# Kernel optimization log

Hardware: AMD Instinct MI355X
Metric: run time of the kernel (lower is better)

## Reference

```python
import jax, jax.numpy as jnp
import numpy as np

N_NODES = 100000
N_EDGES = 1600000
IN_CH, HID, OUT_CH = 512, 32, 64


def setup_inputs() -> dict:
    key = jax.random.key(0)
    ks = jax.random.split(key, 8)
    x = jax.random.normal(ks[0], (N_NODES, IN_CH), dtype=jnp.float32)
    edge_index = jax.random.randint(ks[1], (2, N_EDGES), 0, N_NODES, dtype=jnp.int64)
    def glorot(k, fan_in, fan_out):
        lim = np.sqrt(6.0 / (fan_in + fan_out)).astype(np.float32)
        return jax.random.uniform(k, (fan_in, fan_out), jnp.float32, -lim, lim)
    return {
        "x": x,
        "edge_index": edge_index,
        "W1": glorot(ks[2], IN_CH, HID), "b1": jnp.zeros((HID,), jnp.float32),
        "W2": glorot(ks[3], HID, HID),   "b2": jnp.zeros((HID,), jnp.float32),
        "W3": glorot(ks[4], HID, OUT_CH),"b3": jnp.zeros((OUT_CH,), jnp.float32),
    }


def _gcn_norm(edge_index, n_nodes):
    # PyG GCNConv: add self-loops, symmetric normalization D^-1/2 (A+I) D^-1/2
    loops = jnp.arange(n_nodes, dtype=edge_index.dtype)
    src = jnp.concatenate([edge_index[0], loops])
    dst = jnp.concatenate([edge_index[1], loops])
    deg = jax.ops.segment_sum(jnp.ones_like(dst, dtype=jnp.float32), dst,
                              num_segments=n_nodes)
    dinv = jnp.where(deg > 0, jax.lax.rsqrt(deg), 0.0)
    norm = dinv[src] * dinv[dst]  # [E + N]
    return src, dst, norm


def _gcn_conv(x, W, b, src, dst, norm, n_nodes):
    h = x @ W                                  # [N, F_out] dense GEMM
    msg = h[src] * norm[:, None]               # gather + scale over edges
    out = jax.ops.segment_sum(msg, dst, num_segments=n_nodes)  # scatter-add
    return out + b


def reference(x, edge_index, W1, b1, W2, b2, W3, b3):
    n = x.shape[0]
    src, dst, norm = _gcn_norm(edge_index, n)
    h = _gcn_conv(x, W1, b1, src, dst, norm, n)
    h = jax.nn.relu(h)  # dropout is identity in eval mode (training=False)
    h = _gcn_conv(h, W2, b2, src, dst, norm, n)
    h = jax.nn.relu(h)
    h = _gcn_conv(h, W3, b3, src, dst, norm, n)
    return jax.nn.log_softmax(h, axis=1)
```

## Files before the change

### kernel.cpp

```cpp
#include <hip/hip_runtime.h>
#include <math.h>

static constexpr int NN    = 100000;
static constexpr int NBUCK = (NN + 255) / 256;

#define CDIV(a,b) (((a)+(b)-1)/(b))

typedef __attribute__((ext_vector_type(8))) short bf16x8;
typedef __attribute__((ext_vector_type(4))) float f32x4;

__device__ __forceinline__ float bf2f(unsigned short u) {
    return __uint_as_float(((unsigned)u) << 16);
}
__device__ __forceinline__ unsigned short f2bf(float f) {
    unsigned u = __float_as_uint(f);
    u += 0x7fffu + ((u >> 16) & 1u);
    return (unsigned short)(u >> 16);
}

__global__ __launch_bounds__(512) void k_zero(int* __restrict__ p, int n) {
    int i = blockIdx.x * 512 + threadIdx.x;
    if (i < n) p[i] = 0;
}

__global__ __launch_bounds__(256) void k_wconv(const float* __restrict__ W,
                                               unsigned short* __restrict__ WT) {
    int i = blockIdx.x * 256 + threadIdx.x;
    int k = i >> 5, c = i & 31;
    WT[c * 512 + (((k >> 3) ^ (c & 7)) << 3) + (k & 7)] = f2bf(W[i]);
}

__global__ __launch_bounds__(256) void k_bcount(const int* __restrict__ dst,
                                                int* __restrict__ bcnt,
                                                int E, int chunk) {
    __shared__ int lc[NBUCK];
    for (int i = threadIdx.x; i < NBUCK; i += 256) lc[i] = 0;
    __syncthreads();
    int e0 = blockIdx.x * chunk;
    int e1 = e0 + chunk; if (e1 > E) e1 = E;
    for (int e = e0 + threadIdx.x; e < e1; e += 256)
        atomicAdd(&lc[dst[e] >> 8], 1);
    __syncthreads();
    for (int i = threadIdx.x; i < NBUCK; i += 256)
        if (lc[i]) atomicAdd(&bcnt[i], lc[i]);
}

__global__ __launch_bounds__(512) void k_bscan(const int* __restrict__ bcnt,
                                               int* __restrict__ bbase,
                                               int* __restrict__ bfill, int E) {
    __shared__ int sm[512];
    int t = threadIdx.x;
    int v = (t < NBUCK) ? bcnt[t] : 0;
    sm[t] = v; __syncthreads();
    for (int off = 1; off < 512; off <<= 1) {
        int u = (t >= off) ? sm[t - off] : 0;
        __syncthreads();
        sm[t] += u;
        __syncthreads();
    }
    if (t < NBUCK) { int ex = sm[t] - v; bbase[t] = ex; bfill[t] = ex; }
    if (t == 0) bbase[NBUCK] = E;
}

__global__ __launch_bounds__(256) void k_bpart(const int* __restrict__ src,
                                               const int* __restrict__ dst,
                                               int* __restrict__ bfill,
                                               unsigned int* __restrict__ part,
                                               int E, int chunk) {
    __shared__ int lc[NBUCK];
    __shared__ int boff[NBUCK];
    for (int i = threadIdx.x; i < NBUCK; i += 256) lc[i] = 0;
    __syncthreads();
    int e0 = blockIdx.x * chunk;
    int e1 = e0 + chunk; if (e1 > E) e1 = E;
    for (int e = e0 + threadIdx.x; e < e1; e += 256)
        atomicAdd(&lc[dst[e] >> 8], 1);
    __syncthreads();
    for (int i = threadIdx.x; i < NBUCK; i += 256) {
        int c = lc[i];
        boff[i] = c ? atomicAdd(&bfill[i], c) : 0;
        lc[i] = 0;
    }
    __syncthreads();
    for (int e = e0 + threadIdx.x; e < e1; e += 256) {
        int d = dst[e];
        int b = d >> 8;
        int pos = boff[b] + atomicAdd(&lc[b], 1);
        part[pos] = ((unsigned)src[e] << 8) | (unsigned)(d & 255);
    }
}

__global__ __launch_bounds__(256) void k_bbuild(const unsigned int* __restrict__ part,
                                                const int* __restrict__ bbase,
                                                int* __restrict__ row_ptr,
                                                float* __restrict__ dinv,
                                                int* __restrict__ col, int n, int E) {
    __shared__ int hist[256];
    __shared__ int excl[256];
    __shared__ int fill[256];
    const int b = blockIdx.x;
    const int t = threadIdx.x;
    const int e0 = bbase[b], e1 = bbase[b + 1];
    hist[t] = 0; fill[t] = 0;
    __syncthreads();
    for (int e = e0 + t; e < e1; e += 256)
        atomicAdd(&hist[part[e] & 255], 1);
    __syncthreads();
    int v = hist[t];
    excl[t] = v; __syncthreads();
    for (int off = 1; off < 256; off <<= 1) {
        int u = (t >= off) ? excl[t - off] : 0;
        __syncthreads();
        excl[t] += u;
        __syncthreads();
    }
    int ex = excl[t] - v;
    int g = b * 256 + t;
    if (g < n) {
        row_ptr[g] = e0 + ex;
        dinv[g] = rsqrtf((float)(v + 1));
    }
    if (b == 0 && t == 0) row_ptr[n] = E;
    excl[t] = e0 + ex;
    __syncthreads();
    for (int e = e0 + t; e < e1; e += 256) {
        unsigned u = part[e];
        int ld = u & 255;
        int pos = excl[ld] + atomicAdd(&fill[ld], 1);
        col[pos] = (int)(u >> 8);
    }
}

__global__ __launch_bounds__(256) void k_gemm1(const float* __restrict__ X,
                                               const unsigned short* __restrict__ WT,
                                               const float* __restrict__ dinv,
                                               unsigned short* __restrict__ OUT,
                                               int nrows) {
    __shared__ unsigned short wt[32][512];
    const int t = threadIdx.x;
    {
        const uint4* s = (const uint4*)WT;
        uint4* d = (uint4*)&wt[0][0];
        #pragma unroll
        for (int i = 0; i < 8; i++) d[t + 256 * i] = s[t + 256 * i];
    }
    __syncthreads();

    const int lane  = t & 63;
    const int w     = t >> 6;
    const int grow0 = blockIdx.x * 64 + w * 16;
    const int m     = lane & 15;
    const int kb    = lane >> 4;
    int row = grow0 + m; if (row > nrows - 1) row = nrows - 1;
    const float* xrow = X + (size_t)row * 512 + kb * 8;

    f32x4 acc0 = {0.f, 0.f, 0.f, 0.f};
    f32x4 acc1 = {0.f, 0.f, 0.f, 0.f};
    const int mx  = m & 7;
    const unsigned short* wrow0 = &wt[m][0];
    const unsigned short* wrow1 = &wt[m + 16][0];

    #pragma unroll 4
    for (int kk = 0; kk < 512; kk += 32) {
        float4 xa = *(const float4*)(xrow + kk);
        float4 xb = *(const float4*)(xrow + kk + 4);
        bf16x8 a;
        a[0] = (short)f2bf(xa.x); a[1] = (short)f2bf(xa.y);
        a[2] = (short)f2bf(xa.z); a[3] = (short)f2bf(xa.w);
        a[4] = (short)f2bf(xb.x); a[5] = (short)f2bf(xb.y);
        a[6] = (short)f2bf(xb.z); a[7] = (short)f2bf(xb.w);
        const int g = (kk >> 3) + kb;
        bf16x8 b0 = *(const bf16x8*)&wrow0[((g ^ mx) & 63) * 8];
        bf16x8 b1 = *(const bf16x8*)&wrow1[((g ^ mx) & 63) * 8];
        acc0 = __builtin_amdgcn_mfma_f32_16x16x32_bf16(a, b0, acc0, 0, 0, 0);
        acc1 = __builtin_amdgcn_mfma_f32_16x16x32_bf16(a, b1, acc1, 0, 0, 0);
    }
    #pragma unroll
    for (int j = 0; j < 4; j++) {
        int rr = grow0 + kb * 4 + j;
        if (rr < nrows) {
            float d = dinv[rr];
            OUT[(size_t)rr * 32 + m]      = f2bf(acc0[j] * d);
            OUT[(size_t)rr * 32 + 16 + m] = f2bf(acc1[j] * d);
        }
    }
}

__device__ __forceinline__ float4 agg_gather_bf16(const unsigned short* __restrict__ HS,
                                                  const int* __restrict__ col,
                                                  int s0, int s1, int node, int c0) {
    float4 a0 = {0,0,0,0}, a1 = {0,0,0,0}, a2 = {0,0,0,0}, a3 = {0,0,0,0};
    int e = s0;
    for (; e + 3 < s1; e += 4) {
        int sA = col[e], sB = col[e + 1], sC = col[e + 2], sD = col[e + 3];
        ushort4 uA = *(const ushort4*)&HS[(size_t)sA * 32 + c0];
        ushort4 uB = *(const ushort4*)&HS[(size_t)sB * 32 + c0];
        ushort4 uC = *(const ushort4*)&HS[(size_t)sC * 32 + c0];
        ushort4 uD = *(const ushort4*)&HS[(size_t)sD * 32 + c0];
        a0.x += bf2f(uA.x); a0.y += bf2f(uA.y); a0.z += bf2f(uA.z); a0.w += bf2f(uA.w);
        a1.x += bf2f(uB.x); a1.y += bf2f(uB.y); a1.z += bf2f(uB.z); a1.w += bf2f(uB.w);
        a2.x += bf2f(uC.x); a2.y += bf2f(uC.y); a2.z += bf2f(uC.z); a2.w += bf2f(uC.w);
        a3.x += bf2f(uD.x); a3.y += bf2f(uD.y); a3.z += bf2f(uD.z); a3.w += bf2f(uD.w);
    }
    for (; e < s1; e++) {
        int sA = col[e];
        ushort4 uA = *(const ushort4*)&HS[(size_t)sA * 32 + c0];
        a0.x += bf2f(uA.x); a0.y += bf2f(uA.y); a0.z += bf2f(uA.z); a0.w += bf2f(uA.w);
    }
    ushort4 uS = *(const ushort4*)&HS[(size_t)node * 32 + c0];
    float4 acc;
    acc.x = a0.x + a1.x + a2.x + a3.x + bf2f(uS.x);
    acc.y = a0.y + a1.y + a2.y + a3.y + bf2f(uS.y);
    acc.z = a0.z + a1.z + a2.z + a3.z + bf2f(uS.z);
    acc.w = a0.w + a1.w + a2.w + a3.w + bf2f(uS.w);
    return acc;
}

__global__ __launch_bounds__(256) void k_fuse32(const unsigned short* __restrict__ HS,
                                                const int* __restrict__ row_ptr,
                                                const int* __restrict__ col,
                                                const float* __restrict__ dinv,
                                                const float* __restrict__ bin,
                                                const float* __restrict__ W,
                                                unsigned short* __restrict__ OUT, int n) {
    __shared__ float ws[32][32];
    {
        int i = threadIdx.x;
        int r = i / 8, c = (i % 8) * 4;
        *(float4*)&ws[r][c] = *(const float4*)&W[r * 32 + c];
    }
    __syncthreads();
    const int t    = threadIdx.x;
    const int node = blockIdx.x * 32 + t / 8;
    const int c0   = (t % 8) * 4;
    if (node >= n) return;
    const int s0 = row_ptr[node], s1 = row_ptr[node + 1];
    float4 acc = agg_gather_bf16(HS, col, s0, s1, node, c0);
    const float di = dinv[node];
    float4 b4 = *(const float4*)&bin[c0];
    float4 a;
    a.x = fmaxf(di * acc.x + b4.x, 0.f);
    a.y = fmaxf(di * acc.y + b4.y, 0.f);
    a.z = fmaxf(di * acc.z + b4.z, 0.f);
    a.w = fmaxf(di * acc.w + b4.w, 0.f);
    float4 o = {0,0,0,0};
    const int gb = (t & 63) & ~7;
    #pragma unroll
    for (int s = 0; s < 8; s++) {
        float4 as;
        as.x = __shfl(a.x, gb + s, 64);
        as.y = __shfl(a.y, gb + s, 64);
        as.z = __shfl(a.z, gb + s, 64);
        as.w = __shfl(a.w, gb + s, 64);
        const int k0 = s * 4;
        float4 w0 = *(const float4*)&ws[k0 + 0][c0];
        float4 w1 = *(const float4*)&ws[k0 + 1][c0];
        float4 w2 = *(const float4*)&ws[k0 + 2][c0];
        float4 w3 = *(const float4*)&ws[k0 + 3][c0];
        o.x += as.x*w0.x + as.y*w1.x + as.z*w2.x + as.w*w3.x;
        o.y += as.x*w0.y + as.y*w1.y + as.z*w2.y + as.w*w3.y;
        o.z += as.x*w0.z + as.y*w1.z + as.z*w2.z + as.w*w3.z;
        o.w += as.x*w0.w + as.y*w1.w + as.z*w2.w + as.w*w3.w;
    }
    ushort4 st;
    st.x = f2bf(o.x * di); st.y = f2bf(o.y * di);
    st.z = f2bf(o.z * di); st.w = f2bf(o.w * di);
    *(ushort4*)&OUT[(size_t)node * 32 + c0] = st;
}

__global__ __launch_bounds__(256) void k_aggscale(const unsigned short* __restrict__ HS,
                                                  const int* __restrict__ row_ptr,
                                                  const int* __restrict__ col,
                                                  const float* __restrict__ dinv,
                                                  const float* __restrict__ bin,
                                                  unsigned short* __restrict__ OUT, int n) {
    const int t    = threadIdx.x;
    const int node = blockIdx.x * 32 + t / 8;
    const int c0   = (t % 8) * 4;
    if (node >= n) return;
    const int s0 = row_ptr[node], s1 = row_ptr[node + 1];
    float4 acc = agg_gather_bf16(HS, col, s0, s1, node, c0);
    const float di = dinv[node];
    float4 b4 = *(const float4*)&bin[c0];
    ushort4 o;
    o.x = f2bf(di * fmaxf(di * acc.x + b4.x, 0.f));
    o.y = f2bf(di * fmaxf(di * acc.y + b4.y, 0.f));
    o.z = f2bf(di * fmaxf(di * acc.z + b4.z, 0.f));
    o.w = f2bf(di * fmaxf(di * acc.w + b4.w, 0.f));
    *(ushort4*)&OUT[(size_t)node * 32 + c0] = o;
}

__global__ __launch_bounds__(256) void k_fuseC(const unsigned short* __restrict__ YS,
                                               const int* __restrict__ row_ptr,
                                               const int* __restrict__ col,
                                               const float* __restrict__ dinv,
                                               const float* __restrict__ b3,
                                               const float* __restrict__ W,
                                               float* __restrict__ OUT, int n) {
    __shared__ float ws[32][64];
    {
        int i = threadIdx.x;
        int r0w = i / 16, cw = (i % 16) * 4;
        *(float4*)&ws[r0w][cw]      = *(const float4*)&W[r0w * 64 + cw];
        *(float4*)&ws[r0w + 16][cw] = *(const float4*)&W[(r0w + 16) * 64 + cw];
    }
    __syncthreads();
    const int t    = threadIdx.x;
    const int node = blockIdx.x * 32 + t / 8;
    const int c0   = (t % 8) * 4;
    if (node >= n) return;
    const int s0 = row_ptr[node], s1 = row_ptr[node + 1];
    float4 acc = agg_gather_bf16(YS, col, s0, s1, node, c0);
    const float di = dinv[node];
    float4 g;
    g.x = di * acc.x; g.y = di * acc.y; g.z = di * acc.z; g.w = di * acc.w;
    float4 oL = {0,0,0,0}, oH = {0,0,0,0};
    const int gb = (t & 63) & ~7;
    #pragma unroll
    for (int s = 0; s < 8; s++) {
        float4 gs;
        gs.x = __shfl(g.x, gb + s, 64);
        gs.y = __shfl(g.y, gb + s, 64);
        gs.z = __shfl(g.z, gb + s, 64);
        gs.w = __shfl(g.w, gb + s, 64);
        const int k0 = s * 4;
        #pragma unroll
        for (int q = 0; q < 4; q++) {
            float gv = (q == 0) ? gs.x : (q == 1) ? gs.y : (q == 2) ? gs.z : gs.w;
            float4 wL = *(const float4*)&ws[k0 + q][c0];
            float4 wH = *(const float4*)&ws[k0 + q][32 + c0];
            oL.x += gv * wL.x; oL.y += gv * wL.y; oL.z += gv * wL.z; oL.w += gv * wL.w;
            oH.x += gv * wH.x; oH.y += gv * wH.y; oH.z += gv * wH.z; oH.w += gv * wH.w;
        }
    }
    float4 bL = *(const float4*)&b3[c0];
    float4 bH = *(const float4*)&b3[32 + c0];
    oL.x += bL.x; oL.y += bL.y; oL.z += bL.z; oL.w += bL.w;
    oH.x += bH.x; oH.y += bH.y; oH.z += bH.z; oH.w += bH.w;
    float m = fmaxf(fmaxf(fmaxf(oL.x, oL.y), fmaxf(oL.z, oL.w)),
                    fmaxf(fmaxf(oH.x, oH.y), fmaxf(oH.z, oH.w)));
    #pragma unroll
    for (int off = 1; off < 8; off <<= 1) m = fmaxf(m, __shfl_xor(m, off, 64));
    float sum = expf(oL.x - m) + expf(oL.y - m) + expf(oL.z - m) + expf(oL.w - m)
              + expf(oH.x - m) + expf(oH.y - m) + expf(oH.z - m) + expf(oH.w - m);
    #pragma unroll
    for (int off = 1; off < 8; off <<= 1) sum += __shfl_xor(sum, off, 64);
    float lse = m + logf(sum);
    float4 rL, rH;
    rL.x = oL.x - lse; rL.y = oL.y - lse; rL.z = oL.z - lse; rL.w = oL.w - lse;
    rH.x = oH.x - lse; rH.y = oH.y - lse; rH.z = oH.z - lse; rH.w = oH.w - lse;
    *(float4*)&OUT[(size_t)node * 64 + c0]      = rL;
    *(float4*)&OUT[(size_t)node * 64 + 32 + c0] = rH;
}

extern "C" void kernel_launch(void* const* d_in, const int* in_sizes, int n_in,
                              void* d_out, int out_size, void* d_ws, size_t ws_size,
                              hipStream_t stream) {
    const float* x  = (const float*)d_in[0];
    const int*   ei = (const int*)d_in[1];
    const float* W1 = (const float*)d_in[2];
    const float* b1 = (const float*)d_in[3];
    const float* W2 = (const float*)d_in[4];
    const float* b2 = (const float*)d_in[5];
    const float* W3 = (const float*)d_in[6];
    const float* b3 = (const float*)d_in[7];
    float* out = (float*)d_out;

    const int E = in_sizes[1] / 2;
    const int n = NN;
    const int* src = ei;
    const int* dst = ei + E;

    char* p = (char*)d_ws;
    auto alloc = [&](size_t bytes) -> void* {
        void* r = p;
        p += (bytes + 63) & ~(size_t)63;
        return r;
    };
    int*            bcnt    = (int*)alloc((size_t)NBUCK * 4);
    int*            bbase   = (int*)alloc((size_t)(NBUCK + 1) * 4);
    int*            bfill   = (int*)alloc((size_t)NBUCK * 4);
    unsigned*       part    = (unsigned*)alloc((size_t)E * 4);
    int*            row_ptr = (int*)alloc((size_t)(n + 1) * 4);
    int*            col     = (int*)alloc((size_t)E * 4);
    float*          dinv    = (float*)alloc((size_t)n * 4);
    unsigned short* wtbf    = (unsigned short*)alloc((size_t)512 * 32 * 2);
    unsigned short* hs1     = (unsigned short*)alloc((size_t)n * 32 * 2);
    unsigned short* hs2     = (unsigned short*)alloc((size_t)n * 32 * 2);

    const int NBLK_A = 256;
    const int chunk  = CDIV(E, NBLK_A);

    k_zero<<<1, 512, 0, stream>>>(bcnt, NBUCK);
    k_wconv<<<64, 256, 0, stream>>>(W1, wtbf);
    k_bcount<<<NBLK_A, 256, 0, stream>>>(dst, bcnt, E, chunk);
    k_bscan<<<1, 512, 0, stream>>>(bcnt, bbase, bfill, E);
    k_bpart<<<NBLK_A, 256, 0, stream>>>(src, dst, bfill, part, E, chunk);
    k_bbuild<<<NBUCK, 256, 0, stream>>>(part, bbase, row_ptr, dinv, col, n, E);

    k_gemm1<<<CDIV(n, 64), 256, 0, stream>>>(x, wtbf, dinv, hs1, n);
    k_fuse32<<<CDIV(n, 32), 256, 0, stream>>>(hs1, row_ptr, col, dinv, b1, W2, hs2, n);
    k_aggscale<<<CDIV(n, 32), 256, 0, stream>>>(hs2, row_ptr, col, dinv, b2, hs1, n);
    k_fuseC<<<CDIV(n, 32), 256, 0, stream>>>(hs1, row_ptr, col, dinv, b3, W3, out, n);
}
```

Baseline: 185.4 us.

## Replace atomic bucket offsets with per-block count matrix scan and widen gather unroll

The count kernel now writes per-block bucket counts into a matrix, and the W1 bf16 conversion is folded into it as extra blocks. A new per-bucket scan turns that matrix into deterministic block offsets. This lets the partition kernel skip its second histogram pass and the global atomics, and it also removes the zero and wconv launches. Separately, the edge-gather loop now keeps 8 independent accumulators to put more loads in flight, which costs extra registers.

```diff
diff --git a/kernel.cpp b/kernel.cpp
--- a/kernel.cpp
+++ b/kernel.cpp
@@ -3,6 +3,7 @@
 
 static constexpr int NN    = 100000;
 static constexpr int NBUCK = (NN + 255) / 256;
+static constexpr int NBLK_A = 256;
 
 #define CDIV(a,b) (((a)+(b)-1)/(b))
 
@@ -18,36 +19,54 @@
     return (unsigned short)(u >> 16);
 }
 
-__global__ __launch_bounds__(512) void k_zero(int* __restrict__ p, int n) {
-    int i = blockIdx.x * 512 + threadIdx.x;
-    if (i < n) p[i] = 0;
-}
-
-__global__ __launch_bounds__(256) void k_wconv(const float* __restrict__ W,
-                                               unsigned short* __restrict__ WT) {
-    int i = blockIdx.x * 256 + threadIdx.x;
-    int k = i >> 5, c = i & 31;
-    WT[c * 512 + (((k >> 3) ^ (c & 7)) << 3) + (k & 7)] = f2bf(W[i]);
-}
-
-__global__ __launch_bounds__(256) void k_bcount(const int* __restrict__ dst,
-                                                int* __restrict__ bcnt,
-                                                int E, int chunk) {
+__global__ __launch_bounds__(256) void k_count(const int* __restrict__ dst,
+                                               const float* __restrict__ W1,
+                                               int* __restrict__ gcnt,
+                                               unsigned short* __restrict__ WT,
+                                               int E, int chunk) {
+    const int b = blockIdx.x;
+    const int t = threadIdx.x;
+    if (b >= NBLK_A) {
+        int base = (b - NBLK_A) * 8192 + t;
+        #pragma unroll
+        for (int i = 0; i < 32; i++) {
+            int idx = base + i * 256;
+            int k = idx >> 5, c = idx & 31;
+            WT[c * 512 + (((k >> 3) ^ (c & 7)) << 3) + (k & 7)] = f2bf(W1[idx]);
+        }
+        return;
+    }
     __shared__ int lc[NBUCK];
-    for (int i = threadIdx.x; i < NBUCK; i += 256) lc[i] = 0;
-    __syncthreads();
-    int e0 = blockIdx.x * chunk;
+    for (int i = t; i < NBUCK; i += 256) lc[i] = 0;
+    __syncthreads();
+    int e0 = b * chunk;
     int e1 = e0 + chunk; if (e1 > E) e1 = E;
-    for (int e = e0 + threadIdx.x; e < e1; e += 256)
+    for (int e = e0 + t; e < e1; e += 256)
         atomicAdd(&lc[dst[e] >> 8], 1);
     __syncthreads();
-    for (int i = threadIdx.x; i < NBUCK; i += 256)
-        if (lc[i]) atomicAdd(&bcnt[i], lc[i]);
-}
-
-__global__ __launch_bounds__(512) void k_bscan(const int* __restrict__ bcnt,
-                                               int* __restrict__ bbase,
-                                               int* __restrict__ bfill, int E) {
+    for (int i = t; i < NBUCK; i += 256)
+        gcnt[i * NBLK_A + b] = lc[i];
+}
+
+__global__ __launch_bounds__(256) void k_scan2(const int* __restrict__ gcnt,
+                                               int* __restrict__ gofs,
+                                               int* __restrict__ bcnt) {
+    const int b = blockIdx.x, t = threadIdx.x;
+    __shared__ int sm[256];
+    int v = gcnt[b * NBLK_A + t];
+    sm[t] = v; __syncthreads();
+    for (int off = 1; off < 256; off <<= 1) {
+        int u = (t >= off) ? sm[t - off] : 0;
+        __syncthreads();
+        sm[t] += u;
+        __syncthreads();
+    }
+    gofs[b * NBLK_A + t] = sm[t] - v;
+    if (t == 255) bcnt[b] = sm[255];
+}
+
+__global__ __launch_bounds__(512) void k_scanB(const int* __restrict__ bcnt,
+                                               int* __restrict__ bbase, int E) {
     __shared__ int sm[512];
     int t = threadIdx.x;
     int v = (t < NBUCK) ? bcnt[t] : 0;
@@ -58,30 +77,26 @@
         sm[t] += u;
         __syncthreads();
     }
-    if (t < NBUCK) { int ex = sm[t] - v; bbase[t] = ex; bfill[t] = ex; }
+    if (t < NBUCK) bbase[t] = sm[t] - v;
     if (t == 0) bbase[NBUCK] = E;
 }
 
 __global__ __launch_bounds__(256) void k_bpart(const int* __restrict__ src,
                                                const int* __restrict__ dst,
-                                               int* __restrict__ bfill,
+                                               const int* __restrict__ bbase,
+                                               const int* __restrict__ gofs,
                                                unsigned int* __restrict__ part,
                                                int E, int chunk) {
+    __shared__ int boff[NBUCK];
     __shared__ int lc[NBUCK];
-    __shared__ int boff[NBUCK];
-    for (int i = threadIdx.x; i < NBUCK; i += 256) lc[i] = 0;
-    __syncthreads();
-    int e0 = blockIdx.x * chunk;
+    const int blk = blockIdx.x;
+    for (int i = threadIdx.x; i < NBUCK; i += 256) {
+        boff[i] = bbase[i] + gofs[i * NBLK_A + blk];
+        lc[i] = 0;
+    }
+    __syncthreads();
+    int e0 = blk * chunk;
     int e1 = e0 + chunk; if (e1 > E) e1 = E;
-    for (int e = e0 + threadIdx.x; e < e1; e += 256)
-        atomicAdd(&lc[dst[e] >> 8], 1);
-    __syncthreads();
-    for (int i = threadIdx.x; i < NBUCK; i += 256) {
-        int c = lc[i];
-        boff[i] = c ? atomicAdd(&bfill[i], c) : 0;
-        lc[i] = 0;
-    }
-    __syncthreads();
     for (int e = e0 + threadIdx.x; e < e1; e += 256) {
         int d = dst[e];
         int b = d >> 8;
@@ -189,30 +204,42 @@
 __device__ __forceinline__ float4 agg_gather_bf16(const unsigned short* __restrict__ HS,
                                                   const int* __restrict__ col,
                                                   int s0, int s1, int node, int c0) {
-    float4 a0 = {0,0,0,0}, a1 = {0,0,0,0}, a2 = {0,0,0,0}, a3 = {0,0,0,0};
+    float ax[8], ay[8], az[8], aw[8];
+    #pragma unroll
+    for (int c = 0; c < 8; c++) { ax[c] = ay[c] = az[c] = aw[c] = 0.f; }
     int e = s0;
+    for (; e + 7 < s1; e += 8) {
+        #pragma unroll
+        for (int c = 0; c < 8; c++) {
+            int s = col[e + c];
+            ushort4 u = *(const ushort4*)&HS[(size_t)s * 32 + c0];
+            ax[c] += bf2f(u.x); ay[c] += bf2f(u.y);
+            az[c] += bf2f(u.z); aw[c] += bf2f(u.w);
+        }
+    }
     for (; e + 3 < s1; e += 4) {
-        int sA = col[e], sB = col[e + 1], sC = col[e + 2], sD = col[e + 3];
-        ushort4 uA = *(const ushort4*)&HS[(size_t)sA * 32 + c0];
-        ushort4 uB = *(const ushort4*)&HS[(size_t)sB * 32 + c0];
-        ushort4 uC = *(const ushort4*)&HS[(size_t)sC * 32 + c0];
-        ushort4 uD = *(const ushort4*)&HS[(size_t)sD * 32 + c0];
-        a0.x += bf2f(uA.x); a0.y += bf2f(uA.y); a0.z += bf2f(uA.z); a0.w += bf2f(uA.w);
-        a1.x += bf2f(uB.x); a1.y += bf2f(uB.y); a1.z += bf2f(uB.z); a1.w += bf2f(uB.w);
-        a2.x += bf2f(uC.x); a2.y += bf2f(uC.y); a2.z += bf2f(uC.z); a2.w += bf2f(uC.w);
-        a3.x += bf2f(uD.x); a3.y += bf2f(uD.y); a3.z += bf2f(uD.z); a3.w += bf2f(uD.w);
+        #pragma unroll
+        for (int c = 0; c < 4; c++) {
+            int s = col[e + c];
+            ushort4 u = *(const ushort4*)&HS[(size_t)s * 32 + c0];
+            ax[c] += bf2f(u.x); ay[c] += bf2f(u.y);
+            az[c] += bf2f(u.z); aw[c] += bf2f(u.w);
+        }
     }
     for (; e < s1; e++) {
-        int sA = col[e];
-        ushort4 uA = *(const ushort4*)&HS[(size_t)sA * 32 + c0];
-        a0.x += bf2f(uA.x); a0.y += bf2f(uA.y); a0.z += bf2f(uA.z); a0.w += bf2f(uA.w);
+        int s = col[e];
+        ushort4 u = *(const ushort4*)&HS[(size_t)s * 32 + c0];
+        ax[0] += bf2f(u.x); ay[0] += bf2f(u.y);
+        az[0] += bf2f(u.z); aw[0] += bf2f(u.w);
     }
     ushort4 uS = *(const ushort4*)&HS[(size_t)node * 32 + c0];
+    ax[1] += bf2f(uS.x); ay[1] += bf2f(uS.y);
+    az[1] += bf2f(uS.z); aw[1] += bf2f(uS.w);
     float4 acc;
-    acc.x = a0.x + a1.x + a2.x + a3.x + bf2f(uS.x);
-    acc.y = a0.y + a1.y + a2.y + a3.y + bf2f(uS.y);
-    acc.z = a0.z + a1.z + a2.z + a3.z + bf2f(uS.z);
-    acc.w = a0.w + a1.w + a2.w + a3.w + bf2f(uS.w);
+    acc.x = ((ax[0]+ax[1]) + (ax[2]+ax[3])) + ((ax[4]+ax[5]) + (ax[6]+ax[7]));
+    acc.y = ((ay[0]+ay[1]) + (ay[2]+ay[3])) + ((ay[4]+ay[5]) + (ay[6]+ay[7]));
+    acc.z = ((az[0]+az[1]) + (az[2]+az[3])) + ((az[4]+az[5]) + (az[6]+az[7]));
+    acc.w = ((aw[0]+aw[1]) + (aw[2]+aw[3])) + ((aw[4]+aw[5]) + (aw[6]+aw[7]));
     return acc;
 }
 
@@ -377,9 +404,10 @@
         p += (bytes + 63) & ~(size_t)63;
         return r;
     };
+    int*            gcnt    = (int*)alloc((size_t)NBUCK * NBLK_A * 4);
+    int*            gofs    = (int*)alloc((size_t)NBUCK * NBLK_A * 4);
     int*            bcnt    = (int*)alloc((size_t)NBUCK * 4);
     int*            bbase   = (int*)alloc((size_t)(NBUCK + 1) * 4);
-    int*            bfill   = (int*)alloc((size_t)NBUCK * 4);
     unsigned*       part    = (unsigned*)alloc((size_t)E * 4);
     int*            row_ptr = (int*)alloc((size_t)(n + 1) * 4);
     int*            col     = (int*)alloc((size_t)E * 4);
@@ -388,14 +416,12 @@
     unsigned short* hs1     = (unsigned short*)alloc((size_t)n * 32 * 2);
     unsigned short* hs2     = (unsigned short*)alloc((size_t)n * 32 * 2);
 
-    const int NBLK_A = 256;
-    const int chunk  = CDIV(E, NBLK_A);
-
-    k_zero<<<1, 512, 0, stream>>>(bcnt, NBUCK);
-    k_wconv<<<64, 256, 0, stream>>>(W1, wtbf);
-    k_bcount<<<NBLK_A, 256, 0, stream>>>(dst, bcnt, E, chunk);
-    k_bscan<<<1, 512, 0, stream>>>(bcnt, bbase, bfill, E);
-    k_bpart<<<NBLK_A, 256, 0, stream>>>(src, dst, bfill, part, E, chunk);
+    const int chunk = CDIV(E, NBLK_A);
+
+    k_count<<<NBLK_A + 2, 256, 0, stream>>>(dst, W1, gcnt, wtbf, E, chunk);
+    k_scan2<<<NBUCK, 256, 0, stream>>>(gcnt, gofs, bcnt);
+    k_scanB<<<1, 512, 0, stream>>>(bcnt, bbase, E);
+    k_bpart<<<NBLK_A, 256, 0, stream>>>(src, dst, bbase, gofs, part, E, chunk);
     k_bbuild<<<NBUCK, 256, 0, stream>>>(part, bbase, row_ptr, dinv, col, n, E);
 
     k_gemm1<<<CDIV(n, 64), 256, 0, stream>>>(x, wtbf, dinv, hs1, n);
```

Measured after the change: 190.3 us. +2.6%, slower.
